# Kernel optimization log

Hardware: AMD Instinct MI355X
Metric: run time of the kernel (lower is better)

The kernel has to match this reference:

```python
import jax, jax.numpy as jnp
import numpy as np

EMB = 1024
HEADS = 16
HEAD_DIM = EMB // HEADS
D_FF = 4 * EMB
EPS = 1e-5


def setup_inputs() -> dict:
    key = jax.random.key(0)
    ks = jax.random.split(key, 12)
    b, t = 4, 2048
    sc = 0.02
    return {
        "x": jax.random.normal(ks[0], (b, t, EMB), dtype=jnp.float32),
        # weights stored [in, out] (transpose of torch Linear.weight)
        "w_attn": jax.random.normal(ks[1], (EMB, 3 * EMB), dtype=jnp.float32) * sc,
        "b_attn": jnp.zeros((3 * EMB,), dtype=jnp.float32),
        "w_proj": jax.random.normal(ks[2], (EMB, EMB), dtype=jnp.float32) * sc,
        "b_proj": jnp.zeros((EMB,), dtype=jnp.float32),
        "ln1_g": jnp.ones((EMB,), dtype=jnp.float32),
        "ln1_b": jnp.zeros((EMB,), dtype=jnp.float32),
        "w_ff1": jax.random.normal(ks[3], (EMB, D_FF), dtype=jnp.float32) * sc,
        "b_ff1": jnp.zeros((D_FF,), dtype=jnp.float32),
        "w_ff2": jax.random.normal(ks[4], (D_FF, EMB), dtype=jnp.float32) * sc,
        "b_ff2": jnp.zeros((EMB,), dtype=jnp.float32),
        "ln2_g": jnp.ones((EMB,), dtype=jnp.float32),
        "ln2_b": jnp.zeros((EMB,), dtype=jnp.float32),
    }


def _layernorm(x, g, b):
    mu = jnp.mean(x, axis=-1, keepdims=True)
    var = jnp.var(x, axis=-1, keepdims=True)
    return (x - mu) * jax.lax.rsqrt(var + EPS) * g + b


def reference(x, w_attn, b_attn, w_proj, b_proj, ln1_g, ln1_b,
              w_ff1, b_ff1, w_ff2, b_ff2, ln2_g, ln2_b):
    b, t, e = x.shape
    h, s = HEADS, HEAD_DIM
    # fused qkv projection (GPT2-style c_attn)
    qkv = x @ w_attn + b_attn                      # [b, t, 3e]
    q, k, v = jnp.split(qkv, 3, axis=-1)
    q = q.reshape(b, t, h, s).transpose(0, 2, 1, 3)  # [b, h, t, s]
    k = k.reshape(b, t, h, s).transpose(0, 2, 1, 3)
    v = v.reshape(b, t, h, s).transpose(0, 2, 1, 3)
    dot = jnp.einsum('bhqs,bhks->bhqk', q, k) / jnp.sqrt(jnp.float32(s))
    # causal mask: mask_(..., mask_diagonal=False) zeroes i < j (strict upper)
    causal = jnp.tril(jnp.ones((t, t), dtype=bool))
    dot = jnp.where(causal, dot, jnp.float32(-jnp.inf))
    att = jax.nn.softmax(dot, axis=-1)
    out = jnp.einsum('bhqk,bhks->bhqs', att, v)    # [b, h, t, s]
    out = out.transpose(0, 2, 1, 3).reshape(b, t, e)
    attended = out @ w_proj + b_proj
    # residual + LayerNorm (dropout is identity in eval mode)
    x1 = _layernorm(attended + x, ln1_g, ln1_b)
    ff = jax.nn.relu(x1 @ w_ff1 + b_ff1) @ w_ff2 + b_ff2
    return _layernorm(ff + x1, ln2_g, ln2_b)
```

## Files before the change

### kernel.cpp

```cpp
#include <hip/hip_runtime.h>
#include <hip/hip_bf16.h>


typedef __attribute__((ext_vector_type(8))) short bf16x8;
typedef __attribute__((ext_vector_type(4))) float f32x4;

__device__ __forceinline__ float b2f(unsigned short u) {
  return __uint_as_float(((unsigned int)u) << 16);
}
__device__ __forceinline__ unsigned short f2b(float f) {
  unsigned int u = __float_as_uint(f);
  u += 0x7fffu + ((u >> 16) & 1u);
  return (unsigned short)(u >> 16);
}
__device__ __forceinline__ unsigned int pk2b(float a, float b) {
  __hip_bfloat162 h = __float22bfloat162_rn(make_float2(a, b));
  return *(unsigned int*)&h;
}
__device__ __forceinline__ void gload_lds16(const unsigned short* g, unsigned short* l) {
  __builtin_amdgcn_global_load_lds((const __attribute__((address_space(1))) void*)g,
                                   (__attribute__((address_space(3))) void*)l, 16, 0, 0);
}

__global__ __launch_bounds__(256) void cvt_bf16(const float* __restrict__ in,
                                                unsigned short* __restrict__ out, long n) {
  long i = ((long)blockIdx.x * 256 + threadIdx.x) * 4;
  if (i >= n) return;
  float4 v = *(const float4*)(in + i);
  *(ushort4*)(out + i) = make_ushort4(f2b(v.x), f2b(v.y), f2b(v.z), f2b(v.w));
}

__global__ __launch_bounds__(256) void transpose_bf16(const float* __restrict__ in,
                                                      unsigned short* __restrict__ out,
                                                      int R, int C) {
  __shared__ float tile[32][33];
  int c0 = blockIdx.x * 32, r0 = blockIdx.y * 32;
  for (int i = threadIdx.y; i < 32; i += 8)
    tile[i][threadIdx.x] = in[(long)(r0 + i) * C + c0 + threadIdx.x];
  __syncthreads();
  for (int i = threadIdx.y; i < 32; i += 8)
    out[(long)(c0 + i) * R + r0 + threadIdx.x] = f2b(tile[threadIdx.x][i]);
}

template <int EPI>
__global__ __launch_bounds__(256) void gemm_bf16(const unsigned short* __restrict__ A,
                                                 const unsigned short* __restrict__ Bt,
                                                 const float* __restrict__ bias,
                                                 void* __restrict__ Cout,
                                                 int M, int N, int K) {
  __shared__ unsigned short As[128 * 32];
  __shared__ unsigned short Bs[128 * 32];
  int t = threadIdx.x;
  int bm = blockIdx.x * 128, bn = blockIdx.y * 128;
  int w = t >> 6, lane = t & 63;
  int wr = w >> 1, wc = w & 1, quad = lane >> 4, l16 = lane & 15;
  int srow = t >> 2, scol = (t & 3) * 8;

  const unsigned short* Ap = A + (long)(bm + srow) * K + scol;
  const unsigned short* Bp = Bt + (long)(bn + srow) * K + scol;
  unsigned short* Asw = As + w * 512;
  unsigned short* Bsw = Bs + w * 512;

  f32x4 acc[4][4] = {};

  for (int k0 = 0; k0 < K; k0 += 32) {
    __syncthreads();
    gload_lds16(Ap + k0, Asw);
    gload_lds16(Ap + (long)64 * K + k0, Asw + 2048);
    gload_lds16(Bp + k0, Bsw);
    gload_lds16(Bp + (long)64 * K + k0, Bsw + 2048);
    __syncthreads();
    bf16x8 af[4], bfr[4];
#pragma unroll
    for (int i = 0; i < 4; ++i)
      af[i] = *(const bf16x8*)(As + (wr * 64 + i * 16 + l16) * 32 + quad * 8);
#pragma unroll
    for (int j = 0; j < 4; ++j)
      bfr[j] = *(const bf16x8*)(Bs + (wc * 64 + j * 16 + l16) * 32 + quad * 8);
#pragma unroll
    for (int i = 0; i < 4; ++i)
#pragma unroll
      for (int j = 0; j < 4; ++j)
        acc[i][j] = __builtin_amdgcn_mfma_f32_16x16x32_bf16(af[i], bfr[j], acc[i][j], 0, 0, 0);
  }

#pragma unroll
  for (int i = 0; i < 4; ++i) {
#pragma unroll
    for (int j = 0; j < 4; ++j) {
      int gn = bn + wc * 64 + j * 16 + l16;
      float bv = bias[gn];
      if (EPI == 3 && gn >= 2048) {
        int h = (gn >> 6) & 15, s = gn & 63;
        int gm0 = bm + wr * 64 + i * 16 + quad * 4;
        int b = gm0 >> 11, tt0 = gm0 & 2047;
        unsigned short* vt = (unsigned short*)Cout + 16777216L;
        ushort4 us;
        us.x = f2b(acc[i][j][0] + bv);
        us.y = f2b(acc[i][j][1] + bv);
        us.z = f2b(acc[i][j][2] + bv);
        us.w = f2b(acc[i][j][3] + bv);
        *(ushort4*)(vt + (((long)(b * 16 + h)) * 64 + s) * 2048 + tt0) = us;
      } else {
#pragma unroll
        for (int r = 0; r < 4; ++r) {
          int gm = bm + wr * 64 + i * 16 + quad * 4 + r;
          float v = acc[i][j][r] + bv;
          if (EPI == 2) v = fmaxf(v, 0.f);
          if (EPI == 0) {
            ((float*)Cout)[(long)gm * N + gn] = v;
          } else if (EPI == 1 || EPI == 2) {
            ((unsigned short*)Cout)[(long)gm * N + gn] = f2b(v);
          } else {
            float sc = (gn < 1024) ? 0.18033688011112042f : 1.0f;
            ((unsigned short*)Cout)[(long)gm * 2048 + gn] = f2b(v * sc);
          }
        }
      }
    }
  }
}

__global__ __launch_bounds__(256) void attn_mfma(const unsigned short* __restrict__ qkv,
                                                 unsigned short* __restrict__ outp) {
  const int LD = 72;
  __shared__ __align__(16) unsigned short Ks[64 * LD];
  __shared__ __align__(16) unsigned short Vts[64 * LD];
  __shared__ __align__(16) unsigned short Ps[4][16 * LD];
  int qa = blockIdx.x, qb = 31 - qa;
  int h = blockIdx.y, b = blockIdx.z;
  int t = threadIdx.x;
  int w = t >> 6, lane = t & 63, quad = lane >> 4, l16 = lane & 15;
  const unsigned short* qg = qkv + (long)(b * 2048) * 2048 + h * 64;
  const unsigned short* kg = qg + 1024;
  const unsigned short* vg = qkv + 16777216L + (((long)(b * 16 + h)) * 64) * 2048;
  unsigned short* Pw = &Ps[w][0];

  bf16x8 qfa[2], qfb[2];
#pragma unroll
  for (int ks = 0; ks < 2; ++ks) {
    qfa[ks] = *(const bf16x8*)(qg + (long)(qa * 64 + w * 16 + l16) * 2048 + ks * 32 + quad * 8);
    qfb[ks] = *(const bf16x8*)(qg + (long)(qb * 64 + w * 16 + l16) * 2048 + ks * 32 + quad * 8);
  }

  int sr = t >> 2, sc = (t & 3) * 16;
  const unsigned short* kp = kg + (long)sr * 2048 + sc;
  const unsigned short* vp = vg + (long)sr * 2048 + sc;
  int4 kv0 = *(const int4*)kp, kv1 = *(const int4*)(kp + 8);
  int4 vv0 = *(const int4*)vp, vv1 = *(const int4*)(vp + 8);
  kp += (long)64 * 2048;
  vp += 64;

  f32x4 oa[4] = {}, ob[4] = {};
  f32x4 la = {}, lb = {};
  const short ONE = 0x3F80;
  bf16x8 ones = {ONE, ONE, ONE, ONE, ONE, ONE, ONE, ONE};

  auto process = [&](const bf16x8* qf, int qt, int kt, f32x4* oacc, f32x4& lacc) {
    bool diag = (kt == qt);
#pragma unroll
    for (int rg = 0; rg < 4; ++rg) {
      bf16x8 kf0 = *(const bf16x8*)(Ks + (rg * 16 + l16) * LD + quad * 8);
      bf16x8 kf1 = *(const bf16x8*)(Ks + (rg * 16 + l16) * LD + 32 + quad * 8);
      f32x4 st = {};
      st = __builtin_amdgcn_mfma_f32_16x16x32_bf16(kf0, qf[0], st, 0, 0, 0);
      st = __builtin_amdgcn_mfma_f32_16x16x32_bf16(kf1, qf[1], st, 0, 0, 0);
      if (diag) {
        int kq = rg * 16 + quad * 4;
        int qq = w * 16 + l16;
#pragma unroll
        for (int r = 0; r < 4; ++r)
          if (kq + r > qq) st[r] = -1e30f;
      }
      unsigned int lo = pk2b(exp2f(st[0]), exp2f(st[1]));
      unsigned int hi = pk2b(exp2f(st[2]), exp2f(st[3]));
      *(uint2*)(Pw + l16 * LD + rg * 16 + quad * 4) = make_uint2(lo, hi);
    }
#pragma unroll
    for (int kc = 0; kc < 2; ++kc) {
      bf16x8 ap = *(const bf16x8*)(Pw + l16 * LD + kc * 32 + quad * 8);
      lacc = __builtin_amdgcn_mfma_f32_16x16x32_bf16(ap, ones, lacc, 0, 0, 0);
#pragma unroll
      for (int sg = 0; sg < 4; ++sg) {
        bf16x8 vf = *(const bf16x8*)(Vts + (sg * 16 + l16) * LD + kc * 32 + quad * 8);
        oacc[sg] = __builtin_amdgcn_mfma_f32_16x16x32_bf16(ap, vf, oacc[sg], 0, 0, 0);
      }
    }
  };

  for (int kt = 0; kt <= qb; ++kt) {
    __syncthreads();
    *(int4*)(Ks + sr * LD + sc) = kv0;
    *(int4*)(Ks + sr * LD + sc + 8) = kv1;
    *(int4*)(Vts + sr * LD + sc) = vv0;
    *(int4*)(Vts + sr * LD + sc + 8) = vv1;
    __syncthreads();
    if (kt < qb) {
      kv0 = *(const int4*)kp; kv1 = *(const int4*)(kp + 8);
      vv0 = *(const int4*)vp; vv1 = *(const int4*)(vp + 8);
      kp += (long)64 * 2048;
      vp += 64;
    }
    process(qfb, qb, kt, ob, lb);
    if (kt <= qa) process(qfa, qa, kt, oa, la);
  }

  auto epi = [&](int qt, f32x4* oacc, f32x4& lacc) {
#pragma unroll
    for (int r = 0; r < 4; ++r) {
      float invl = 1.f / lacc[r];
      int row = qt * 64 + w * 16 + quad * 4 + r;
      unsigned short* op = outp + ((long)(b * 2048 + row)) * 1024 + h * 64;
#pragma unroll
      for (int sg = 0; sg < 4; ++sg) op[sg * 16 + l16] = f2b(oacc[sg][r] * invl);
    }
  };
  epi(qa, oa, la);
  epi(qb, ob, lb);
}

__global__ __launch_bounds__(256) void ln_kernel(const float* __restrict__ a,
                                                 const float* __restrict__ res,
                                                 const float* __restrict__ gam,
                                                 const float* __restrict__ bet,
                                                 float* __restrict__ outf,
                                                 unsigned short* __restrict__ outb) {
  int row = blockIdx.x, t = threadIdx.x;
  float4 av = *(const float4*)(a + (long)row * 1024 + t * 4);
  float4 rv = *(const float4*)(res + (long)row * 1024 + t * 4);
  float v0 = av.x + rv.x, v1 = av.y + rv.y, v2 = av.z + rv.z, v3 = av.w + rv.w;
  float s = v0 + v1 + v2 + v3;
  float ss = v0 * v0 + v1 * v1 + v2 * v2 + v3 * v3;
#pragma unroll
  for (int off = 32; off >= 1; off >>= 1) {
    s += __shfl_down(s, off);
    ss += __shfl_down(ss, off);
  }
  __shared__ float sb[4], ssb[4];
  __shared__ float mean_s, inv_s;
  int w = t >> 6, lane = t & 63;
  if (lane == 0) { sb[w] = s; ssb[w] = ss; }
  __syncthreads();
  if (t == 0) {
    float S = sb[0] + sb[1] + sb[2] + sb[3];
    float SS = ssb[0] + ssb[1] + ssb[2] + ssb[3];
    float mean = S * (1.f / 1024.f);
    float var = SS * (1.f / 1024.f) - mean * mean;
    mean_s = mean;
    inv_s = rsqrtf(var + 1e-5f);
  }
  __syncthreads();
  float mean = mean_s, inv = inv_s;
  int c = t * 4;
  float4 gv = *(const float4*)(gam + c);
  float4 bv = *(const float4*)(bet + c);
  float y0 = (v0 - mean) * inv * gv.x + bv.x;
  float y1 = (v1 - mean) * inv * gv.y + bv.y;
  float y2 = (v2 - mean) * inv * gv.z + bv.z;
  float y3 = (v3 - mean) * inv * gv.w + bv.w;
  *(float4*)(outf + (long)row * 1024 + c) = make_float4(y0, y1, y2, y3);
  if (outb) {
    *(ushort4*)(outb + (long)row * 1024 + c) = make_ushort4(f2b(y0), f2b(y1), f2b(y2), f2b(y3));
  }
}

extern "C" void kernel_launch(void* const* d_in, const int* in_sizes, int n_in,
                              void* d_out, int out_size, void* d_ws, size_t ws_size,
                              hipStream_t stream) {
  const float* x      = (const float*)d_in[0];
  const float* w_attn = (const float*)d_in[1];
  const float* b_attn = (const float*)d_in[2];
  const float* w_proj = (const float*)d_in[3];
  const float* b_proj = (const float*)d_in[4];
  const float* ln1_g  = (const float*)d_in[5];
  const float* ln1_b  = (const float*)d_in[6];
  const float* w_ff1  = (const float*)d_in[7];
  const float* b_ff1  = (const float*)d_in[8];
  const float* w_ff2  = (const float*)d_in[9];
  const float* b_ff2  = (const float*)d_in[10];
  const float* ln2_g  = (const float*)d_in[11];
  const float* ln2_b  = (const float*)d_in[12];

  const long M = 8192, E = 1024;
  char* ws = (char*)d_ws;
  unsigned short* xb   = (unsigned short*)ws; ws += M * E * 2;
  unsigned short* wTa  = (unsigned short*)ws; ws += 3072L * 1024 * 2;
  unsigned short* wTp  = (unsigned short*)ws; ws += 1024L * 1024 * 2;
  unsigned short* wTf1 = (unsigned short*)ws; ws += 4096L * 1024 * 2;
  unsigned short* wTf2 = (unsigned short*)ws; ws += 4096L * 1024 * 2;
  unsigned short* qkvb = (unsigned short*)ws; ws += M * 3072 * 2;
  unsigned short* attb = (unsigned short*)ws; ws += M * E * 2;
  float* a1f = (float*)ws; ws += M * E * 4;
  float* x1f = (float*)ws; ws += M * E * 4;
  unsigned short* x1b = (unsigned short*)ws; ws += M * E * 2;
  unsigned short* hb = qkvb;
  float* f2 = a1f;

  cvt_bf16<<<dim3((M * E) / 4 / 256), dim3(256), 0, stream>>>(x, xb, M * E);
  transpose_bf16<<<dim3(3072 / 32, 1024 / 32), dim3(32, 8), 0, stream>>>(w_attn, wTa, 1024, 3072);
  transpose_bf16<<<dim3(1024 / 32, 1024 / 32), dim3(32, 8), 0, stream>>>(w_proj, wTp, 1024, 1024);
  transpose_bf16<<<dim3(4096 / 32, 1024 / 32), dim3(32, 8), 0, stream>>>(w_ff1, wTf1, 1024, 4096);
  transpose_bf16<<<dim3(1024 / 32, 4096 / 32), dim3(32, 8), 0, stream>>>(w_ff2, wTf2, 4096, 1024);
  gemm_bf16<3><<<dim3(64, 24), dim3(256), 0, stream>>>(xb, wTa, b_attn, qkvb, 8192, 3072, 1024);
  attn_mfma<<<dim3(16, 16, 4), dim3(256), 0, stream>>>(qkvb, attb);
  gemm_bf16<0><<<dim3(64, 8), dim3(256), 0, stream>>>(attb, wTp, b_proj, a1f, 8192, 1024, 1024);
  ln_kernel<<<dim3(8192), dim3(256), 0, stream>>>(a1f, x, ln1_g, ln1_b, x1f, x1b);
  gemm_bf16<2><<<dim3(64, 32), dim3(256), 0, stream>>>(x1b, wTf1, b_ff1, hb, 8192, 4096, 1024);
  gemm_bf16<0><<<dim3(64, 8), dim3(256), 0, stream>>>(hb, wTf2, b_ff2, f2, 8192, 1024, 4096);
  ln_kernel<<<dim3(8192), dim3(256), 0, stream>>>(f2, x1f, ln2_g, ln2_b, (float*)d_out, nullptr);
}
```

Baseline: 569.9 us.

## Split-K the N=1024 GEMMs and fuse partial-sum reduction into LayerNorm

Adds a split-K grid dimension to the bf16 GEMM and uses it with two K chunks for the attention-output projection and the second feed-forward GEMM. Those GEMMs launch only 512 tiles, so this doubles the number of blocks to fill the GPU better. The second chunk writes an fp32 partial sum, without bias, into buffers that are no longer needed (the qkv buffer and the front of the workspace). The LayerNorm kernel reads the extra partial and adds it, which costs additional fp32 write and read traffic in exchange for more parallelism.

```diff
diff --git a/kernel.cpp b/kernel.cpp
--- a/kernel.cpp
+++ b/kernel.cpp
@@ -47,17 +47,19 @@
                                                  const unsigned short* __restrict__ Bt,
                                                  const float* __restrict__ bias,
                                                  void* __restrict__ Cout,
-                                                 int M, int N, int K) {
+                                                 void* __restrict__ Cout2,
+                                                 int M, int N, int K, int Kstride) {
   __shared__ unsigned short As[128 * 32];
   __shared__ unsigned short Bs[128 * 32];
   int t = threadIdx.x;
   int bm = blockIdx.x * 128, bn = blockIdx.y * 128;
+  int chunk = blockIdx.z;
   int w = t >> 6, lane = t & 63;
   int wr = w >> 1, wc = w & 1, quad = lane >> 4, l16 = lane & 15;
   int srow = t >> 2, scol = (t & 3) * 8;
 
-  const unsigned short* Ap = A + (long)(bm + srow) * K + scol;
-  const unsigned short* Bp = Bt + (long)(bn + srow) * K + scol;
+  const unsigned short* Ap = A + (long)(bm + srow) * Kstride + (long)chunk * K + scol;
+  const unsigned short* Bp = Bt + (long)(bn + srow) * Kstride + (long)chunk * K + scol;
   unsigned short* Asw = As + w * 512;
   unsigned short* Bsw = Bs + w * 512;
 
@@ -66,9 +68,9 @@
   for (int k0 = 0; k0 < K; k0 += 32) {
     __syncthreads();
     gload_lds16(Ap + k0, Asw);
-    gload_lds16(Ap + (long)64 * K + k0, Asw + 2048);
+    gload_lds16(Ap + (long)64 * Kstride + k0, Asw + 2048);
     gload_lds16(Bp + k0, Bsw);
-    gload_lds16(Bp + (long)64 * K + k0, Bsw + 2048);
+    gload_lds16(Bp + (long)64 * Kstride + k0, Bsw + 2048);
     __syncthreads();
     bf16x8 af[4], bfr[4];
 #pragma unroll
@@ -84,12 +86,13 @@
         acc[i][j] = __builtin_amdgcn_mfma_f32_16x16x32_bf16(af[i], bfr[j], acc[i][j], 0, 0, 0);
   }
 
+  void* Cbase = chunk ? Cout2 : Cout;
 #pragma unroll
   for (int i = 0; i < 4; ++i) {
 #pragma unroll
     for (int j = 0; j < 4; ++j) {
       int gn = bn + wc * 64 + j * 16 + l16;
-      float bv = bias[gn];
+      float bv = chunk ? 0.f : bias[gn];
       if (EPI == 3 && gn >= 2048) {
         int h = (gn >> 6) & 15, s = gn & 63;
         int gm0 = bm + wr * 64 + i * 16 + quad * 4;
@@ -108,12 +111,12 @@
           float v = acc[i][j][r] + bv;
           if (EPI == 2) v = fmaxf(v, 0.f);
           if (EPI == 0) {
-            ((float*)Cout)[(long)gm * N + gn] = v;
+            ((float*)Cbase)[(long)gm * N + gn] = v;
           } else if (EPI == 1 || EPI == 2) {
-            ((unsigned short*)Cout)[(long)gm * N + gn] = f2b(v);
+            ((unsigned short*)Cbase)[(long)gm * N + gn] = f2b(v);
           } else {
             float sc = (gn < 1024) ? 0.18033688011112042f : 1.0f;
-            ((unsigned short*)Cout)[(long)gm * 2048 + gn] = f2b(v * sc);
+            ((unsigned short*)Cbase)[(long)gm * 2048 + gn] = f2b(v * sc);
           }
         }
       }
@@ -220,6 +223,7 @@
 }
 
 __global__ __launch_bounds__(256) void ln_kernel(const float* __restrict__ a,
+                                                 const float* __restrict__ a2,
                                                  const float* __restrict__ res,
                                                  const float* __restrict__ gam,
                                                  const float* __restrict__ bet,
@@ -229,6 +233,10 @@
   float4 av = *(const float4*)(a + (long)row * 1024 + t * 4);
   float4 rv = *(const float4*)(res + (long)row * 1024 + t * 4);
   float v0 = av.x + rv.x, v1 = av.y + rv.y, v2 = av.z + rv.z, v3 = av.w + rv.w;
+  if (a2) {
+    float4 a2v = *(const float4*)(a2 + (long)row * 1024 + t * 4);
+    v0 += a2v.x; v1 += a2v.y; v2 += a2v.z; v3 += a2v.w;
+  }
   float s = v0 + v1 + v2 + v3;
   float ss = v0 * v0 + v1 * v1 + v2 * v2 + v3 * v3;
 #pragma unroll
@@ -295,17 +303,19 @@
   unsigned short* x1b = (unsigned short*)ws; ws += M * E * 2;
   unsigned short* hb = qkvb;
   float* f2 = a1f;
+  float* prj1 = (float*)qkvb;
+  float* ff21 = (float*)d_ws;
 
   cvt_bf16<<<dim3((M * E) / 4 / 256), dim3(256), 0, stream>>>(x, xb, M * E);
   transpose_bf16<<<dim3(3072 / 32, 1024 / 32), dim3(32, 8), 0, stream>>>(w_attn, wTa, 1024, 3072);
   transpose_bf16<<<dim3(1024 / 32, 1024 / 32), dim3(32, 8), 0, stream>>>(w_proj, wTp, 1024, 1024);
   transpose_bf16<<<dim3(4096 / 32, 1024 / 32), dim3(32, 8), 0, stream>>>(w_ff1, wTf1, 1024, 4096);
   transpose_bf16<<<dim3(1024 / 32, 4096 / 32), dim3(32, 8), 0, stream>>>(w_ff2, wTf2, 4096, 1024);
-  gemm_bf16<3><<<dim3(64, 24), dim3(256), 0, stream>>>(xb, wTa, b_attn, qkvb, 8192, 3072, 1024);
+  gemm_bf16<3><<<dim3(64, 24, 1), dim3(256), 0, stream>>>(xb, wTa, b_attn, qkvb, nullptr, 8192, 3072, 1024, 1024);
   attn_mfma<<<dim3(16, 16, 4), dim3(256), 0, stream>>>(qkvb, attb);
-  gemm_bf16<0><<<dim3(64, 8), dim3(256), 0, stream>>>(attb, wTp, b_proj, a1f, 8192, 1024, 1024);
-  ln_kernel<<<dim3(8192), dim3(256), 0, stream>>>(a1f, x, ln1_g, ln1_b, x1f, x1b);
-  gemm_bf16<2><<<dim3(64, 32), dim3(256), 0, stream>>>(x1b, wTf1, b_ff1, hb, 8192, 4096, 1024);
-  gemm_bf16<0><<<dim3(64, 8), dim3(256), 0, stream>>>(hb, wTf2, b_ff2, f2, 8192, 1024, 4096);
-  ln_kernel<<<dim3(8192), dim3(256), 0, stream>>>(f2, x1f, ln2_g, ln2_b, (float*)d_out, nullptr);
-}
+  gemm_bf16<0><<<dim3(64, 8, 2), dim3(256), 0, stream>>>(attb, wTp, b_proj, a1f, prj1, 8192, 1024, 512, 1024);
+  ln_kernel<<<dim3(8192), dim3(256), 0, stream>>>(a1f, prj1, x, ln1_g, ln1_b, x1f, x1b);
+  gemm_bf16<2><<<dim3(64, 32, 1), dim3(256), 0, stream>>>(x1b, wTf1, b_ff1, hb, nullptr, 8192, 4096, 1024, 1024);
+  gemm_bf16<0><<<dim3(64, 8, 2), dim3(256), 0, stream>>>(hb, wTf2, b_ff2, f2, ff21, 8192, 1024, 2048, 4096);
+  ln_kernel<<<dim3(8192), dim3(256), 0, stream>>>(f2, ff21, x1f, ln2_g, ln2_b, (float*)d_out, nullptr);
+}
```

Result: slower. 607.4 us (+6.6%).
